# Performance work log

Hardware: AMD Instinct MI355X
Metric: run time of the kernel (lower is better)

Reference implementation:

```python
import jax, jax.numpy as jnp
import numpy as np

B, S, E, H = 2, 2048, 1024, 16
Dh = E // H  # 64
KEEP = 0.9   # 1 - dropout_p
INV_SCALE = 1.0  # forward() default; call site does not pass inv_scale


def setup_inputs() -> dict:
    key = jax.random.key(0)
    ks = jax.random.split(key, 12)
    query = jax.random.normal(ks[0], (B, S, E), dtype=jnp.float32)
    key_t = jax.random.normal(ks[1], (B, S, E), dtype=jnp.float32)
    value = jax.random.normal(ks[2], (B, S, E), dtype=jnp.float32)
    attn_mask = jax.random.randint(ks[3], (B, S), 0, 2, dtype=jnp.int32)
    # pre-scaled inverted dropout keep-mask (deterministic stand-in for F.dropout)
    dropout_mask = (jax.random.uniform(ks[4], (B, H, S, S)) < KEEP).astype(jnp.float32) / KEEP
    Wq = jax.random.normal(ks[5], (E, E), dtype=jnp.float32) * 0.02
    bq = jnp.zeros((E,), dtype=jnp.float32)
    Wk = jax.random.normal(ks[6], (E, E), dtype=jnp.float32) * 0.02
    bk = jnp.zeros((E,), dtype=jnp.float32)
    Wv = jax.random.normal(ks[7], (E, E), dtype=jnp.float32) * 0.02
    bv = jnp.zeros((E,), dtype=jnp.float32)
    return {"query": query, "key": key_t, "value": value, "attn_mask": attn_mask,
            "dropout_mask": dropout_mask, "Wq": Wq, "bq": bq, "Wk": Wk, "bk": bk,
            "Wv": Wv, "bv": bv}


def _heads(x, W, b):
    # Linear then split heads: (B,S,E) -> (B,H,S,Dh)
    y = x @ W.T + b
    return y.reshape(B, S, H, Dh).transpose(0, 2, 1, 3)


def reference(query, key, value, attn_mask, dropout_mask, Wq, bq, Wk, bk, Wv, bv):
    q = _heads(query, Wq, bq)
    k = _heads(key, Wk, bk)
    v = _heads(value, Wv, bv)
    scores = jnp.einsum("bhqd,bhkd->bhqk", q, k) / INV_SCALE
    pad = (attn_mask == 0)[:, None, None, :]  # (B,1,1,S) True = masked
    scores = jnp.where(pad, -jnp.inf, scores)
    attn = jax.nn.softmax(scores, axis=-1) * dropout_mask
    out = jnp.einsum("bhqk,bhkd->bhqd", attn, v)  # (B,H,S,Dh)
    return out
```

## Files before the change

### kernel.cpp

```cpp
#include <hip/hip_runtime.h>

#define B_ 2
#define S_ 2048
#define E_ 1024
#define H_ 16
#define DH 64
#define MM (B_*S_)
#define BHN (B_*H_)
#define KSPLIT 4

typedef unsigned short u16;
typedef unsigned int u32;
typedef __attribute__((ext_vector_type(8))) __bf16 bf16x8;
typedef __attribute__((ext_vector_type(8))) _Float16 f16x8;
typedef __attribute__((ext_vector_type(4))) float f32x4;
typedef __attribute__((ext_vector_type(8))) u16 u16x8;
typedef __attribute__((ext_vector_type(4))) u16 u16x4;

static __device__ __forceinline__ u16 f2bf(float f) {
  u32 u = __builtin_bit_cast(u32, f);
  u += 0x7fffu + ((u >> 16) & 1u);
  return (u16)(u >> 16);
}
static __device__ __forceinline__ float bf2f(u16 h) {
  return __builtin_bit_cast(float, (u32)h << 16);
}
static __device__ __forceinline__ u32 sw(u32 byte) {
  return byte ^ (((byte >> 7) & 7u) << 4);
}
static __device__ __forceinline__ bf16x8 frag(const u16* lds, u32 byte) {
  return *(const bf16x8*)((const char*)lds + byte);
}
static __device__ __forceinline__ f16x8 frag16(const u16* lds, u32 byte) {
  return *(const f16x8*)((const char*)lds + byte);
}
static __device__ __forceinline__ f32x4 mfma_bf(bf16x8 a, bf16x8 b, f32x4 c) {
  return __builtin_amdgcn_mfma_f32_16x16x32_bf16(a, b, c, 0, 0, 0);
}
static __device__ __forceinline__ f32x4 mfma_f16(f16x8 a, f16x8 b, f32x4 c) {
  return __builtin_amdgcn_mfma_f32_16x16x32_f16(a, b, c, 0, 0, 0);
}
static __device__ __forceinline__ void gload_lds16(const void* g, void* lds_base) {
  __builtin_amdgcn_global_load_lds(
      (const __attribute__((address_space(1))) u32*)g,
      (__attribute__((address_space(3))) u32*)lds_base, 16, 0, 0);
}

#define L2E 1.44269504088896340736f

struct SplitArg { const float* s; u16* h; u16* l; int n4; };

__global__ void split6_kernel(SplitArg a0, SplitArg a1, SplitArg a2,
                              SplitArg a3, SplitArg a4, SplitArg a5) {
  SplitArg A = (blockIdx.z == 0) ? a0 : (blockIdx.z == 1) ? a1 : (blockIdx.z == 2) ? a2
             : (blockIdx.z == 3) ? a3 : (blockIdx.z == 4) ? a4 : a5;
  int i = blockIdx.x * blockDim.x + threadIdx.x;
  int stride = gridDim.x * blockDim.x;
  if (A.l) {
    for (; i < A.n4; i += stride) {
      float4 v = ((const float4*)A.s)[i];
      u16x4 h, l;
      h.x = f2bf(v.x); l.x = f2bf(v.x - bf2f(h.x));
      h.y = f2bf(v.y); l.y = f2bf(v.y - bf2f(h.y));
      h.z = f2bf(v.z); l.z = f2bf(v.z - bf2f(h.z));
      h.w = f2bf(v.w); l.w = f2bf(v.w - bf2f(h.w));
      ((u16x4*)A.h)[i] = h;
      ((u16x4*)A.l)[i] = l;
    }
  } else {
    for (; i < A.n4; i += stride) {
      float4 v = ((const float4*)A.s)[i];
      u16x4 h;
      h.x = f2bf(v.x); h.y = f2bf(v.y); h.z = f2bf(v.z); h.w = f2bf(v.w);
      ((u16x4*)A.h)[i] = h;
    }
  }
}

__global__ void pack_mask(const int* __restrict__ am, u32* __restrict__ pm) {
  int w = threadIdx.x;
  if (w < 128) {
    int base = (w >> 6) * 2048 + (w & 63) * 32;
    u32 bits = 0;
#pragma unroll
    for (int j = 0; j < 8; ++j) {
      int4 v = *(const int4*)(am + base + j * 4);
      bits |= (v.x ? 1u : 0u) << (4 * j) | (v.y ? 1u : 0u) << (4 * j + 1) |
              (v.z ? 1u : 0u) << (4 * j + 2) | (v.w ? 1u : 0u) << (4 * j + 3);
    }
    pm[w] = bits;
  }
}

struct ProjArgs {
  const u16* xhi; const u16* xlo; const u16* whi; const u16* wlo;
  const float* bias; u16* ohi; int mode;
};

__global__ __launch_bounds__(256, 3) void proj_gemm(ProjArgs a0, ProjArgs a1, ProjArgs a2) {
  ProjArgs A = (blockIdx.z == 0) ? a0 : (blockIdx.z == 1) ? a1 : a2;
  __shared__ u16 As[128 * 64];
  __shared__ u16 Bs[128 * 64];
  const int t = threadIdx.x;
  const int l = t & 63, wid = t >> 6;
  const int g = l >> 4, ln = l & 15;
  const int wm = wid >> 1, wn = wid & 1;
  int bid = blockIdx.y * 8 + blockIdx.x;
  int sid = (bid & 7) * 32 + (bid >> 3);
  const int m0 = (sid >> 3) * 128, e0 = (sid & 7) * 128;

  f32x4 acc[4][4] = {};
  const int nkt = (A.mode == 2) ? 32 : 48;

  for (int kt = 0; kt < nkt; ++kt) {
    int kp = kt * 64;
    const u16* asrc = (kp < 2048) ? A.xhi : A.xlo;
    const u16* bsrc = (kp < 1024 || kp >= 2048) ? A.whi : A.wlo;
    int kc = kp & 1023;
#pragma unroll
    for (int r = 0; r < 4; ++r) {
      int cr = wid * 4 + r;
      int row = cr * 8 + (l >> 3);
      int col = (l & 7) * 8;
      gload_lds16(asrc + (size_t)(m0 + row) * 1024 + kc + col, As + cr * 512);
      gload_lds16(bsrc + (size_t)(e0 + row) * 1024 + kc + col, Bs + cr * 512);
    }
    __syncthreads();
#pragma unroll
    for (int ks = 0; ks < 2; ++ks) {
      bf16x8 af[4], bfv[4];
#pragma unroll
      for (int i = 0; i < 4; ++i) {
        af[i] = frag(As, (u32)(wm * 64 + i * 16 + ln) * 128 + ks * 64 + g * 16);
        bfv[i] = frag(Bs, (u32)(wn * 64 + i * 16 + ln) * 128 + ks * 64 + g * 16);
      }
#pragma unroll
      for (int i = 0; i < 4; ++i)
#pragma unroll
        for (int j = 0; j < 4; ++j)
          acc[i][j] = mfma_bf(af[i], bfv[j], acc[i][j]);
    }
    __syncthreads();
  }

#pragma unroll
  for (int i = 0; i < 4; ++i) {
#pragma unroll
    for (int j = 0; j < 4; ++j) {
      int e = e0 + wn * 64 + j * 16 + ln;
      int h = e >> 6, d = e & 63;
      float bias = A.bias[e];
      if (A.mode < 2) {
#pragma unroll
        for (int r = 0; r < 4; ++r) {
          int m = m0 + wm * 64 + i * 16 + g * 4 + r;
          float v = acc[i][j][r] + bias;
          if (A.mode == 0) v *= L2E;
          int b = m >> 11, s = m & 2047;
          size_t idx = ((size_t)((b * 16 + h) * 2048 + s)) * 64 + d;
          A.ohi[idx] = __builtin_bit_cast(u16, (_Float16)v);
        }
      } else {
        int m = m0 + wm * 64 + i * 16 + g * 4;
        int b = m >> 11, s = m & 2047;
        u16x4 pv;
#pragma unroll
        for (int r = 0; r < 4; ++r)
          pv[r] = __builtin_bit_cast(u16, (__bf16)(acc[i][j][r] + bias));
        size_t idx = ((size_t)((b * 16 + h) * 64 + d)) * 2048 + s;
        *(u16x4*)(A.ohi + idx) = pv;
      }
    }
  }
}

__global__ __launch_bounds__(256, 2) void attn_kernel(
    const u16* __restrict__ qf, const u16* __restrict__ kf,
    const u16* __restrict__ vt, const u32* __restrict__ pm,
    const float* __restrict__ dmask, float* __restrict__ opart,
    float* __restrict__ zpart) {
  __shared__ u16 Ks[2][64 * 64];
  __shared__ u16 Vs[2][64 * 64];
  __shared__ float Dm[2][64 * 64];
  __shared__ u16 Ps[4 * 16 * 64];

  const int t = threadIdx.x, l = t & 63, wid = t >> 6;
  const int g = l >> 4, ln = l & 15;

  int bid = blockIdx.y * 32 + blockIdx.x;
  int sid = (bid & 7) * 128 + (bid >> 3);
  const int qt = sid & 31, bh = sid >> 5, b = bh >> 4;
  const int kc = blockIdx.z;
  const int q0 = qt * 64;
  const int qrow = q0 + wid * 16 + ln;
  const size_t qg = ((size_t)bh * 2048 + qrow) * 64;
  const u32* pmb = pm + b * 64;

  f16x8 qv[2];
#pragma unroll
  for (int ks = 0; ks < 2; ++ks)
    qv[ks] = *(const f16x8*)(qf + qg + ks * 32 + g * 8);

  const int c0 = wid * 64 + l, c1 = wid * 64 + 256 + l;
  const int s0 = c0 ^ ((c0 >> 3) & 7), s1 = c1 ^ ((c1 >> 3) & 7);
  const u16* kp0 = kf + (size_t)bh * 2048 * 64 + s0 * 8;
  const u16* kp1 = kf + (size_t)bh * 2048 * 64 + s1 * 8;
  const u16* vp0 = vt + ((size_t)bh * 64 + (s0 >> 3)) * 2048 + (s0 & 7) * 8;
  const u16* vp1 = vt + ((size_t)bh * 64 + (s1 >> 3)) * 2048 + (s1 & 7) * 8;

  const float* dmbase = dmask + ((size_t)bh * 2048 + q0) * 2048;
  int dmrowq[4]; int dmcolq[4];
#pragma unroll
  for (int r = 0; r < 4; ++r) {
    int c = r * 256 + t;
    dmrowq[r] = c >> 4;
    dmcolq[r] = ((c & 15) ^ ((c >> 4) & 7)) * 4;
  }

  auto stage_tile = [&](int buf, int kt2) {
    gload_lds16(kp0 + (size_t)kt2 * 4096, Ks[buf] + (wid * 64) * 8);
    gload_lds16(kp1 + (size_t)kt2 * 4096, Ks[buf] + (wid * 64 + 256) * 8);
    gload_lds16(vp0 + kt2 * 64, Vs[buf] + (wid * 64) * 8);
    gload_lds16(vp1 + kt2 * 64, Vs[buf] + (wid * 64 + 256) * 8);
    const float* dsrc = dmbase + kt2 * 64;
#pragma unroll
    for (int r = 0; r < 4; ++r)
      gload_lds16(dsrc + (size_t)dmrowq[r] * 2048 + dmcolq[r],
                  Dm[buf] + (r * 256 + t) * 4);
  };

  const int kt2_last = kc * 8 + 7;

  stage_tile(0, kc * 8);

  f32x4 O[4] = {};
  float Zacc = 0.f;
  const u32 psbase = (u32)(wid * 2048 + ln * 128);
  u32 pw[4], pr[2], dmoff[4];
#pragma unroll
  for (int i = 0; i < 4; ++i) pw[i] = sw(psbase + i * 32 + g * 8);
#pragma unroll
  for (int ks = 0; ks < 2; ++ks) pr[ks] = sw(psbase + ks * 64 + g * 16);
#pragma unroll
  for (int i = 0; i < 4; ++i)
    dmoff[i] = (u32)(((wid * 16 + ln) * 256 + i * 64 + g * 16) ^ ((ln & 7) << 4));

  for (int kt = 0; kt < 8; ++kt) {
    const int buf = kt & 1;
    const int kt2 = kc * 8 + kt;
    const int ktn = (kt < 7) ? kt2 + 1 : kt2_last;

    __builtin_amdgcn_s_barrier();
    __builtin_amdgcn_sched_barrier(0);

    stage_tile(buf ^ 1, ktn);

    asm volatile("s_waitcnt vmcnt(8)" ::: "memory");
    __builtin_amdgcn_sched_barrier(0);
    __builtin_amdgcn_s_barrier();
    __builtin_amdgcn_sched_barrier(0);

    u32 m0 = pmb[2 * kt2], m1 = pmb[2 * kt2 + 1];

    f32x4 sc[4] = {};
#pragma unroll
    for (int ks = 0; ks < 2; ++ks) {
#pragma unroll
      for (int i = 0; i < 4; ++i) {
        f16x8 ak = frag16(Ks[buf], sw((u32)((i * 16 + ln) * 128 + ks * 64 + g * 16)));
        sc[i] = mfma_f16(ak, qv[ks], sc[i]);
      }
    }

#pragma unroll
    for (int i = 0; i < 4; ++i) {
      f32x4 dm = *(const f32x4*)((const char*)Dm[buf] + dmoff[i]);
      u32 mm = (i < 2 ? m0 : m1) >> (((i & 1) << 4) + 4 * g);
      float e0 = (mm & 1u) ? exp2f(sc[i][0]) : 0.f;
      float e1 = (mm & 2u) ? exp2f(sc[i][1]) : 0.f;
      float e2 = (mm & 4u) ? exp2f(sc[i][2]) : 0.f;
      float e3 = (mm & 8u) ? exp2f(sc[i][3]) : 0.f;
      Zacc += (e0 + e1) + (e2 + e3);
      u16x4 p;
      p.x = __builtin_bit_cast(u16, (__bf16)(e0 * dm[0]));
      p.y = __builtin_bit_cast(u16, (__bf16)(e1 * dm[1]));
      p.z = __builtin_bit_cast(u16, (__bf16)(e2 * dm[2]));
      p.w = __builtin_bit_cast(u16, (__bf16)(e3 * dm[3]));
      *(u16x4*)((char*)Ps + pw[i]) = p;
    }

#pragma unroll
    for (int ks = 0; ks < 2; ++ks) {
      bf16x8 bP = frag(Ps, pr[ks]);
#pragma unroll
      for (int id = 0; id < 4; ++id) {
        bf16x8 aV = frag(Vs[buf], sw((u32)((id * 16 + ln) * 128 + ks * 64 + g * 16)));
        O[id] = mfma_bf(aV, bP, O[id]);
      }
    }
  }

  float z = Zacc;
  z += __shfl_xor(z, 16, 64);
  z += __shfl_xor(z, 32, 64);
  const int row = bh * 2048 + qrow;
  if (g == 0) zpart[kc * (BHN * S_) + row] = z;

  float* opb = opart + ((size_t)kc * (BHN * S_) + row) * 64;
#pragma unroll
  for (int id = 0; id < 4; ++id) {
    float4 o;
    o.x = O[id][0]; o.y = O[id][1]; o.z = O[id][2]; o.w = O[id][3];
    *(float4*)(opb + id * 16 + 4 * g) = o;
  }
}

__global__ void combine_kernel(const float* __restrict__ op,
                               const float* __restrict__ zp,
                               float* __restrict__ out) {
  int tid = blockIdx.x * blockDim.x + threadIdx.x;
  int row = tid >> 4, d4 = tid & 15;
  float4 o = make_float4(0.f, 0.f, 0.f, 0.f);
  float z = 0.f;
#pragma unroll
  for (int kc = 0; kc < KSPLIT; ++kc) {
    float4 v = *(const float4*)(op + ((size_t)kc * (BHN * S_) + row) * 64 + d4 * 4);
    o.x += v.x; o.y += v.y; o.z += v.z; o.w += v.w;
    z += zp[kc * (BHN * S_) + row];
  }
  float rz = 1.f / z;
  float4 r;
  r.x = o.x * rz; r.y = o.y * rz; r.z = o.z * rz; r.w = o.w * rz;
  *(float4*)(out + (size_t)row * 64 + d4 * 4) = r;
}

extern "C" void kernel_launch(void* const* d_in, const int* in_sizes, int n_in,
                              void* d_out, int out_size, void* d_ws, size_t ws_size,
                              hipStream_t stream) {
  const float* query = (const float*)d_in[0];
  const float* keyt  = (const float*)d_in[1];
  const float* value = (const float*)d_in[2];
  const int*   amask = (const int*)d_in[3];
  const float* dmask = (const float*)d_in[4];
  const float* Wq = (const float*)d_in[5];
  const float* bq = (const float*)d_in[6];
  const float* Wk = (const float*)d_in[7];
  const float* bk = (const float*)d_in[8];
  const float* Wv = (const float*)d_in[9];
  const float* bv = (const float*)d_in[10];

  char* ws = (char*)d_ws;
  size_t off = 0;
  auto alloc = [&](size_t bytes) {
    char* p = ws + off;
    off += (bytes + 255) & ~(size_t)255;
    return p;
  };
  const size_t XB = (size_t)MM * E_ * sizeof(u16);
  const size_t WB = (size_t)E_ * E_ * sizeof(u16);

  u16 *xh[3], *xl[3], *wh[3], *wl[3];
  for (int i = 0; i < 3; ++i) { xh[i] = (u16*)alloc(XB); xl[i] = (u16*)alloc(XB); }
  for (int i = 0; i < 3; ++i) { wh[i] = (u16*)alloc(WB); wl[i] = (u16*)alloc(WB); }
  u16* q_f16 = (u16*)alloc(XB);
  u16* k_f16 = (u16*)alloc(XB);
  u16* v_t   = (u16*)alloc(XB);
  u32* pmask = (u32*)alloc(512);
  float* opart = (float*)alloc((size_t)KSPLIT * BHN * S_ * 64 * 4);
  float* zpart = (float*)alloc((size_t)KSPLIT * BHN * S_ * 4);
  if (off > ws_size) return;

  SplitArg sa[6] = {
      {query, xh[0], xl[0], MM * E_ / 4}, {keyt, xh[1], xl[1], MM * E_ / 4},
      {value, xh[2], nullptr, MM * E_ / 4}, {Wq, wh[0], wl[0], E_ * E_ / 4},
      {Wk, wh[1], wl[1], E_ * E_ / 4},    {Wv, wh[2], wl[2], E_ * E_ / 4},
  };
  split6_kernel<<<dim3(512, 1, 6), 256, 0, stream>>>(sa[0], sa[1], sa[2], sa[3], sa[4], sa[5]);
  pack_mask<<<1, 128, 0, stream>>>(amask, pmask);

  ProjArgs pa[3] = {
      {xh[0], xl[0], wh[0], wl[0], bq, q_f16, 0},
      {xh[1], xl[1], wh[1], wl[1], bk, k_f16, 1},
      {xh[2], nullptr, wh[2], wl[2], bv, v_t, 2},
  };
  proj_gemm<<<dim3(8, 32, 3), 256, 0, stream>>>(pa[0], pa[1], pa[2]);

  attn_kernel<<<dim3(32, 32, KSPLIT), 256, 0, stream>>>(
      q_f16, k_f16, v_t, pmask, dmask, opart, zpart);

  combine_kernel<<<(BHN * S_ * 64 / 4) / 256, 256, 0, stream>>>(
      opart, zpart, (float*)d_out);
}
```

Before: 289.2 us.

## Pre-pack dropout mask to bits inside projection launch and drop LDS staging

Adds a fourth z-slice to the projection GEMM launch. That slice uses wave ballots to compress the fp32 dropout mask into one bit per element. The attention kernel then reads a single 64-bit word per row per tile instead of staging a 64x64 fp32 tile through LDS. The 1/keep scale is folded into the final combine. Freeing that LDS lets the attention kernel raise its occupancy bound from 2 to 3. The full fp32 mask is still read once, now with narrow scalar loads inside a launch shared with the GEMM. The packing assumes every mask value is either 0 or exactly 1/0.9.

```diff
diff --git a/kernel.cpp b/kernel.cpp
--- a/kernel.cpp
+++ b/kernel.cpp
@@ -11,6 +11,7 @@
 
 typedef unsigned short u16;
 typedef unsigned int u32;
+typedef unsigned long long u64;
 typedef __attribute__((ext_vector_type(8))) __bf16 bf16x8;
 typedef __attribute__((ext_vector_type(8))) _Float16 f16x8;
 typedef __attribute__((ext_vector_type(4))) float f32x4;
@@ -47,6 +48,7 @@
 }
 
 #define L2E 1.44269504088896340736f
+#define INV_KEEP 1.1111112f
 
 struct SplitArg { const float* s; u16* h; u16* l; int n4; };
 
@@ -97,12 +99,31 @@
   const float* bias; u16* ohi; int mode;
 };
 
-__global__ __launch_bounds__(256, 3) void proj_gemm(ProjArgs a0, ProjArgs a1, ProjArgs a2) {
+__global__ __launch_bounds__(256, 3) void proj_gemm(ProjArgs a0, ProjArgs a1, ProjArgs a2,
+                                                    const float* __restrict__ dmask,
+                                                    u64* __restrict__ db) {
+  const int t = threadIdx.x;
+  const int l = t & 63, wid = t >> 6;
+
+  if (blockIdx.z == 3) {
+    int wgid = (blockIdx.y * 8 + blockIdx.x) * 4 + wid;
+    for (int j = 0; j < 64; ++j) {
+      size_t row = (size_t)wgid * 64 + j;
+      const float* src = dmask + row * 2048 + l;
+      u64* dst = db + row * 32;
+#pragma unroll 4
+      for (int c = 0; c < 32; ++c) {
+        float v = src[c * 64];
+        u64 bits = __ballot(v > 0.f);
+        if (l == 0) dst[c] = bits;
+      }
+    }
+    return;
+  }
+
   ProjArgs A = (blockIdx.z == 0) ? a0 : (blockIdx.z == 1) ? a1 : a2;
   __shared__ u16 As[128 * 64];
   __shared__ u16 Bs[128 * 64];
-  const int t = threadIdx.x;
-  const int l = t & 63, wid = t >> 6;
   const int g = l >> 4, ln = l & 15;
   const int wm = wid >> 1, wn = wid & 1;
   int bid = blockIdx.y * 8 + blockIdx.x;
@@ -174,14 +195,13 @@
   }
 }
 
-__global__ __launch_bounds__(256, 2) void attn_kernel(
+__global__ __launch_bounds__(256, 3) void attn_kernel(
     const u16* __restrict__ qf, const u16* __restrict__ kf,
     const u16* __restrict__ vt, const u32* __restrict__ pm,
-    const float* __restrict__ dmask, float* __restrict__ opart,
+    const u64* __restrict__ db, float* __restrict__ opart,
     float* __restrict__ zpart) {
   __shared__ u16 Ks[2][64 * 64];
   __shared__ u16 Vs[2][64 * 64];
-  __shared__ float Dm[2][64 * 64];
   __shared__ u16 Ps[4 * 16 * 64];
 
   const int t = threadIdx.x, l = t & 63, wid = t >> 6;
@@ -195,6 +215,7 @@
   const int qrow = q0 + wid * 16 + ln;
   const size_t qg = ((size_t)bh * 2048 + qrow) * 64;
   const u32* pmb = pm + b * 64;
+  const u64* dbq = db + ((size_t)bh * 2048 + qrow) * 32;
 
   f16x8 qv[2];
 #pragma unroll
@@ -208,42 +229,24 @@
   const u16* vp0 = vt + ((size_t)bh * 64 + (s0 >> 3)) * 2048 + (s0 & 7) * 8;
   const u16* vp1 = vt + ((size_t)bh * 64 + (s1 >> 3)) * 2048 + (s1 & 7) * 8;
 
-  const float* dmbase = dmask + ((size_t)bh * 2048 + q0) * 2048;
-  int dmrowq[4]; int dmcolq[4];
-#pragma unroll
-  for (int r = 0; r < 4; ++r) {
-    int c = r * 256 + t;
-    dmrowq[r] = c >> 4;
-    dmcolq[r] = ((c & 15) ^ ((c >> 4) & 7)) * 4;
-  }
-
   auto stage_tile = [&](int buf, int kt2) {
     gload_lds16(kp0 + (size_t)kt2 * 4096, Ks[buf] + (wid * 64) * 8);
     gload_lds16(kp1 + (size_t)kt2 * 4096, Ks[buf] + (wid * 64 + 256) * 8);
     gload_lds16(vp0 + kt2 * 64, Vs[buf] + (wid * 64) * 8);
     gload_lds16(vp1 + kt2 * 64, Vs[buf] + (wid * 64 + 256) * 8);
-    const float* dsrc = dmbase + kt2 * 64;
-#pragma unroll
-    for (int r = 0; r < 4; ++r)
-      gload_lds16(dsrc + (size_t)dmrowq[r] * 2048 + dmcolq[r],
-                  Dm[buf] + (r * 256 + t) * 4);
   };
 
   const int kt2_last = kc * 8 + 7;
-
   stage_tile(0, kc * 8);
 
   f32x4 O[4] = {};
   float Zacc = 0.f;
   const u32 psbase = (u32)(wid * 2048 + ln * 128);
-  u32 pw[4], pr[2], dmoff[4];
+  u32 pw[4], pr[2];
 #pragma unroll
   for (int i = 0; i < 4; ++i) pw[i] = sw(psbase + i * 32 + g * 8);
 #pragma unroll
   for (int ks = 0; ks < 2; ++ks) pr[ks] = sw(psbase + ks * 64 + g * 16);
-#pragma unroll
-  for (int i = 0; i < 4; ++i)
-    dmoff[i] = (u32)(((wid * 16 + ln) * 256 + i * 64 + g * 16) ^ ((ln & 7) << 4));
 
   for (int kt = 0; kt < 8; ++kt) {
     const int buf = kt & 1;
@@ -255,11 +258,12 @@
 
     stage_tile(buf ^ 1, ktn);
 
-    asm volatile("s_waitcnt vmcnt(8)" ::: "memory");
+    asm volatile("s_waitcnt vmcnt(4)" ::: "memory");
     __builtin_amdgcn_sched_barrier(0);
     __builtin_amdgcn_s_barrier();
     __builtin_amdgcn_sched_barrier(0);
 
+    u64 w = dbq[kt2];
     u32 m0 = pmb[2 * kt2], m1 = pmb[2 * kt2 + 1];
 
     f32x4 sc[4] = {};
@@ -272,20 +276,22 @@
       }
     }
 
+    u32 blo = (u32)w, bhi = (u32)(w >> 32);
 #pragma unroll
     for (int i = 0; i < 4; ++i) {
-      f32x4 dm = *(const f32x4*)((const char*)Dm[buf] + dmoff[i]);
-      u32 mm = (i < 2 ? m0 : m1) >> (((i & 1) << 4) + 4 * g);
-      float e0 = (mm & 1u) ? exp2f(sc[i][0]) : 0.f;
-      float e1 = (mm & 2u) ? exp2f(sc[i][1]) : 0.f;
-      float e2 = (mm & 4u) ? exp2f(sc[i][2]) : 0.f;
-      float e3 = (mm & 8u) ? exp2f(sc[i][3]) : 0.f;
+      u32 sh = ((i & 1) << 4) + 4 * g;
+      u32 pd = (i < 2 ? m0 : m1) >> sh;
+      u32 dr = (i < 2 ? blo : bhi) >> sh;
+      float e0 = (pd & 1u) ? exp2f(sc[i][0]) : 0.f;
+      float e1 = (pd & 2u) ? exp2f(sc[i][1]) : 0.f;
+      float e2 = (pd & 4u) ? exp2f(sc[i][2]) : 0.f;
+      float e3 = (pd & 8u) ? exp2f(sc[i][3]) : 0.f;
       Zacc += (e0 + e1) + (e2 + e3);
       u16x4 p;
-      p.x = __builtin_bit_cast(u16, (__bf16)(e0 * dm[0]));
-      p.y = __builtin_bit_cast(u16, (__bf16)(e1 * dm[1]));
-      p.z = __builtin_bit_cast(u16, (__bf16)(e2 * dm[2]));
-      p.w = __builtin_bit_cast(u16, (__bf16)(e3 * dm[3]));
+      p.x = (dr & 1u) ? __builtin_bit_cast(u16, (__bf16)e0) : (u16)0;
+      p.y = (dr & 2u) ? __builtin_bit_cast(u16, (__bf16)e1) : (u16)0;
+      p.z = (dr & 4u) ? __builtin_bit_cast(u16, (__bf16)e2) : (u16)0;
+      p.w = (dr & 8u) ? __builtin_bit_cast(u16, (__bf16)e3) : (u16)0;
       *(u16x4*)((char*)Ps + pw[i]) = p;
     }
 
@@ -328,7 +334,7 @@
     o.x += v.x; o.y += v.y; o.z += v.z; o.w += v.w;
     z += zp[kc * (BHN * S_) + row];
   }
-  float rz = 1.f / z;
+  float rz = INV_KEEP / z;
   float4 r;
   r.x = o.x * rz; r.y = o.y * rz; r.z = o.z * rz; r.w = o.w * rz;
   *(float4*)(out + (size_t)row * 64 + d4 * 4) = r;
@@ -366,6 +372,7 @@
   u16* k_f16 = (u16*)alloc(XB);
   u16* v_t   = (u16*)alloc(XB);
   u32* pmask = (u32*)alloc(512);
+  u64* dbits = (u64*)alloc((size_t)BHN * S_ * 32 * 8);
   float* opart = (float*)alloc((size_t)KSPLIT * BHN * S_ * 64 * 4);
   float* zpart = (float*)alloc((size_t)KSPLIT * BHN * S_ * 4);
   if (off > ws_size) return;
@@ -383,10 +390,10 @@
       {xh[1], xl[1], wh[1], wl[1], bk, k_f16, 1},
       {xh[2], nullptr, wh[2], wl[2], bv, v_t, 2},
   };
-  proj_gemm<<<dim3(8, 32, 3), 256, 0, stream>>>(pa[0], pa[1], pa[2]);
+  proj_gemm<<<dim3(8, 32, 4), 256, 0, stream>>>(pa[0], pa[1], pa[2], dmask, dbits);
 
   attn_kernel<<<dim3(32, 32, KSPLIT), 256, 0, stream>>>(
-      q_f16, k_f16, v_t, pmask, dmask, opart, zpart);
+      q_f16, k_f16, v_t, pmask, dbits, opart, zpart);
 
   combine_kernel<<<(BHN * S_ * 64 / 4) / 256, 256, 0, stream>>>(
       opart, zpart, (float*)d_out);
```

New measurement: 1.105 ms. +282.0%, slower.
